# Kernel optimization log

Hardware: AMD Instinct MI355X
Metric: run time of the kernel (lower is better)

The kernel has to match this reference:

```python
import jax, jax.numpy as jnp
import numpy as np

B, S, H, QKV, NH, MLP = 4, 2048, 512, 512, 8, 2048
HD = QKV // NH
EPS = 1e-6


def _layernorm(x):
    # LayerNorm over last dim, no affine, eps=1e-6
    mu = jnp.mean(x, axis=-1, keepdims=True)
    var = jnp.mean(jnp.square(x - mu), axis=-1, keepdims=True)
    return (x - mu) * jax.lax.rsqrt(var + EPS)


def setup_inputs() -> dict:
    key = jax.random.key(0)
    ks = jax.random.split(key, 8)
    sc_in = 1.0 / np.sqrt(H)
    sc_qkv = 1.0 / np.sqrt(QKV)
    sc_mlp = 1.0 / np.sqrt(MLP)
    return {
        "input": jax.random.normal(ks[0], (B, S, H), dtype=jnp.float32),
        "mask": jnp.ones((B, S), dtype=jnp.float32),
        "Wq": jax.random.normal(ks[1], (H, QKV), dtype=jnp.float32) * sc_in,
        "Wk": jax.random.normal(ks[2], (H, QKV), dtype=jnp.float32) * sc_in,
        "Wv": jax.random.normal(ks[3], (H, QKV), dtype=jnp.float32) * sc_in,
        "Wo": jax.random.normal(ks[4], (QKV, H), dtype=jnp.float32) * sc_qkv,
        "W1": jax.random.normal(ks[5], (H, MLP), dtype=jnp.float32) * sc_in,
        "W2": jax.random.normal(ks[6], (MLP, H), dtype=jnp.float32) * sc_mlp,
    }


def reference(input, mask, Wq, Wk, Wv, Wo, W1, W2):
    # pre-mask + pre-norm
    x = input * mask[..., None]
    x = _layernorm(x)
    # qkv projections, split heads: [B,S,QKV] -> [B,NH,S,HD]
    def heads(t):
        return t.reshape(B, S, NH, HD).transpose(0, 2, 1, 3)
    q = heads(x @ Wq) * (1.0 / np.sqrt(HD))
    k = heads(x @ Wk)
    v = heads(x @ Wv)
    logits = jnp.einsum("bhqd,bhkd->bhqk", q, k)  # [B,NH,S,S]
    amask = mask[:, None, :, None]  # 'b q -> b 1 q 1'
    logits = logits + (-100000.0) * (1.0 - amask)
    att = jax.nn.softmax(logits, axis=-1)
    out = jnp.einsum("bhqk,bhkd->bhqd", att, v)
    out = out.transpose(0, 2, 1, 3).reshape(B, S, QKV)
    x = input + out @ Wo  # residual
    x = x * mask[..., None]
    y = _layernorm(x)
    ffn = jax.nn.gelu(y @ W1, approximate=False) @ W2
    return ffn + x
```

## Files before the change

kernel.cpp:

```cpp
#include <hip/hip_runtime.h>
#include <hip/hip_bf16.h>
#include <cmath>

typedef __attribute__((ext_vector_type(8))) short bf16x8;
typedef __attribute__((ext_vector_type(4))) short u16x4;
typedef __attribute__((ext_vector_type(4))) float f32x4;
typedef __attribute__((ext_vector_type(16))) float f32x16;
typedef unsigned short u16;
typedef unsigned int u32;

#define B_ 4
#define S_ 2048
#define H_ 512
#define NH_ 8
#define HD_ 64
#define MLP_ 2048
#define M_ (B_*S_)
#define LOG2E 1.44269504088896340736f

__device__ __forceinline__ float bf2f(u16 u){ u32 v=((u32)u)<<16; float f; __builtin_memcpy(&f,&v,4); return f; }
__device__ __forceinline__ u16 f2bf(float f){ u32 u; __builtin_memcpy(&u,&f,4); u32 r=(u+0x7fffu+((u>>16)&1u))>>16; return (u16)r; }
__device__ __forceinline__ u32 pk2(float lo, float hi2){
  __hip_bfloat162 t = __float22bfloat162_rn(make_float2(lo, hi2));
  u32 r; __builtin_memcpy(&r, &t, 4); return r;
}

__device__ __forceinline__ float xhalf_add(float x){
  float a = x, b = x;
  asm volatile("v_permlane32_swap_b32 %0, %1" : "+v"(a), "+v"(b));
  return a + b;
}

__device__ __forceinline__ void gl16(const u16* g, u16* l) {
  __builtin_amdgcn_global_load_lds((const __attribute__((address_space(1))) u32*)(g),
                                   (__attribute__((address_space(3))) u32*)(l), 16, 0, 0);
}

__device__ __forceinline__ void gemm_core(
    const u16* __restrict__ A, const u16* __restrict__ Bt,
    int lda, int ldb, int nkt, int m0, int n0,
    u16* As, u16* Bs, f32x4 (&acc)[4][4])
{
  const int tid = threadIdx.x;
  const int lane = tid & 63;
  const int w = tid >> 6;
  const int lr = lane & 15;
  const int g  = lane >> 4;
  const int wr = w >> 1, wc = w & 1;

  const int sr = lane >> 3;
  const int scol = ((lane & 7) ^ sr) << 3;

  int aoff[2][4], boff[2][4];
#pragma unroll
  for (int m = 0; m < 4; ++m) {
    int ra = wr*64 + m*16 + lr;
    int rb = wc*64 + m*16 + lr;
#pragma unroll
    for (int kk = 0; kk < 2; ++kk) {
      aoff[kk][m] = ra*64 + (((kk*4+g) ^ (ra&7))<<3);
      boff[kk][m] = rb*64 + (((kk*4+g) ^ (rb&7))<<3);
    }
  }
  const u16* Ap = A + (size_t)m0*lda;
  const u16* Bp = Bt + (size_t)n0*ldb;

#pragma unroll
  for (int c = 0; c < 4; ++c) {
    gl16(Ap + (size_t)(w*32 + c*8 + sr)*lda + scol, As + w*2048 + c*512);
    gl16(Bp + (size_t)(w*32 + c*8 + sr)*ldb + scol, Bs + w*2048 + c*512);
  }

  for (int kt = 0; kt < nkt; ++kt) {
    const int cb = (kt & 1) * 8192;
    if (kt + 1 < nkt) {
      const int k0 = (kt + 1) << 6;
      const int nb = ((kt + 1) & 1) * 8192;
#pragma unroll
      for (int c = 0; c < 4; ++c) {
        gl16(Ap + (size_t)(w*32 + c*8 + sr)*lda + k0 + scol, As + nb + w*2048 + c*512);
        gl16(Bp + (size_t)(w*32 + c*8 + sr)*ldb + k0 + scol, Bs + nb + w*2048 + c*512);
      }
      asm volatile("s_waitcnt vmcnt(8)" ::: "memory");
    } else {
      asm volatile("s_waitcnt vmcnt(0)" ::: "memory");
    }
    __builtin_amdgcn_s_barrier();

#pragma unroll
    for (int kk = 0; kk < 2; ++kk) {
      bf16x8 af[4], bfr[4];
#pragma unroll
      for (int m = 0; m < 4; ++m) {
        af[m]  = *(const bf16x8*)(As + cb + aoff[kk][m]);
        bfr[m] = *(const bf16x8*)(Bs + cb + boff[kk][m]);
      }
#pragma unroll
      for (int m = 0; m < 4; ++m) {
#pragma unroll
        for (int n = 0; n < 4; ++n) {
          acc[m][n] = __builtin_amdgcn_mfma_f32_16x16x32_bf16(af[m], bfr[n], acc[m][n], 0, 0, 0);
        }
      }
    }
    __builtin_amdgcn_s_barrier();
  }
}

__device__ __forceinline__ void gemm_core64(
    const u16* __restrict__ A, const u16* __restrict__ Bt,
    int lda, int ldb, int nkt, int m0, int n0,
    u16* As, u16* Bs, f32x4 (&acc)[2][4])
{
  const int tid = threadIdx.x;
  const int lane = tid & 63;
  const int w = tid >> 6;
  const int lr = lane & 15;
  const int g  = lane >> 4;

  const int sr = lane >> 3;
  const int scol = ((lane & 7) ^ sr) << 3;

  int aoff[2][2], boff[2][4];
#pragma unroll
  for (int m = 0; m < 2; ++m) {
    int ra = w*32 + m*16 + lr;
#pragma unroll
    for (int kk = 0; kk < 2; ++kk) aoff[kk][m] = ra*64 + (((kk*4+g) ^ (ra&7))<<3);
  }
#pragma unroll
  for (int n = 0; n < 4; ++n) {
    int rb = n*16 + lr;
#pragma unroll
    for (int kk = 0; kk < 2; ++kk) boff[kk][n] = rb*64 + (((kk*4+g) ^ (rb&7))<<3);
  }
  const u16* Ap = A + (size_t)m0*lda;
  const u16* Bp = Bt + (size_t)n0*ldb;

#pragma unroll
  for (int c = 0; c < 4; ++c)
    gl16(Ap + (size_t)(w*32 + c*8 + sr)*lda + scol, As + w*2048 + c*512);
#pragma unroll
  for (int c = 0; c < 2; ++c)
    gl16(Bp + (size_t)(w*16 + c*8 + sr)*ldb + scol, Bs + w*1024 + c*512);

  for (int kt = 0; kt < nkt; ++kt) {
    const int cbA = (kt & 1) * 8192;
    const int cbB = (kt & 1) * 4096;
    if (kt + 1 < nkt) {
      const int k0 = (kt + 1) << 6;
      const int nbA = ((kt + 1) & 1) * 8192;
      const int nbB = ((kt + 1) & 1) * 4096;
#pragma unroll
      for (int c = 0; c < 4; ++c)
        gl16(Ap + (size_t)(w*32 + c*8 + sr)*lda + k0 + scol, As + nbA + w*2048 + c*512);
#pragma unroll
      for (int c = 0; c < 2; ++c)
        gl16(Bp + (size_t)(w*16 + c*8 + sr)*ldb + k0 + scol, Bs + nbB + w*1024 + c*512);
      asm volatile("s_waitcnt vmcnt(6)" ::: "memory");
    } else {
      asm volatile("s_waitcnt vmcnt(0)" ::: "memory");
    }
    __builtin_amdgcn_s_barrier();

#pragma unroll
    for (int kk = 0; kk < 2; ++kk) {
      bf16x8 af[2], bfr[4];
#pragma unroll
      for (int m = 0; m < 2; ++m) af[m] = *(const bf16x8*)(As + cbA + aoff[kk][m]);
#pragma unroll
      for (int n = 0; n < 4; ++n) bfr[n] = *(const bf16x8*)(Bs + cbB + boff[kk][n]);
#pragma unroll
      for (int m = 0; m < 2; ++m) {
#pragma unroll
        for (int n = 0; n < 4; ++n) {
          acc[m][n] = __builtin_amdgcn_mfma_f32_16x16x32_bf16(af[m], bfr[n], acc[m][n], 0, 0, 0);
        }
      }
    }
    __builtin_amdgcn_s_barrier();
  }
}

__global__ __launch_bounds__(256,2) void k_qkv(
    const u16* __restrict__ xn, const u16* __restrict__ wqt,
    const u16* __restrict__ wkt, const u16* __restrict__ wvt,
    u16* __restrict__ q, u16* __restrict__ k, u16* __restrict__ vt)
{
  __shared__ u16 As[2*128*64], Bs[2*128*64];
  int m0 = blockIdx.x*128;
  int sel = blockIdx.y >> 2;
  int n0 = (blockIdx.y & 3)*128;
  const u16* Bt = sel==0 ? wqt : (sel==1 ? wkt : wvt);
  float alpha = (sel==0) ? 0.125f*LOG2E : 1.0f;
  f32x4 acc[4][4] = {};
  gemm_core(xn, Bt, H_, H_, H_/64, m0, n0, As, Bs, acc);
  const int lane = threadIdx.x&63, w = threadIdx.x>>6;
  const int lr = lane&15, g = lane>>4, wr = w>>1, wc = w&1;
  if (sel == 2) {
#pragma unroll
    for (int m=0;m<4;++m) {
#pragma unroll
      for (int n=0;n<4;++n) {
        int rowb = m0 + wr*64 + m*16 + g*4;
        int col  = n0 + wc*64 + n*16 + lr;
        int b = rowb >> 11, s = rowb & 2047;
        int h = col >> 6, d = col & 63;
        u16x4 t;
#pragma unroll
        for (int r=0;r<4;++r) t[r] = (short)f2bf(acc[m][n][r]);
        *(u16x4*)(vt + ((size_t)((b*NH_ + h)*HD_ + d))*S_ + s) = t;
      }
    }
  } else {
    u16* O = sel==0 ? q : k;
#pragma unroll
    for (int m=0;m<4;++m) {
#pragma unroll
      for (int n=0;n<4;++n) {
#pragma unroll
        for (int r=0;r<4;++r) {
          int row = m0 + wr*64 + m*16 + g*4 + r;
          int col = n0 + wc*64 + n*16 + lr;
          O[(size_t)row*H_ + col] = f2bf(acc[m][n][r]*alpha);
        }
      }
    }
  }
}

template<int EPI>
__global__ __launch_bounds__(256,2) void k_gemm(
    const u16* __restrict__ A, const u16* __restrict__ Bt, void* __restrict__ Ov,
    const float* __restrict__ aux, const float* __restrict__ maskv,
    int N, int K)
{
  __shared__ u16 As[2*128*64], Bs[2*128*64];
  int m0 = blockIdx.x*128, n0 = blockIdx.y*128;
  f32x4 acc[4][4] = {};
  gemm_core(A, Bt, K, K, K>>6, m0, n0, As, Bs, acc);
  const int lane = threadIdx.x&63, w = threadIdx.x>>6;
  const int lr = lane&15, g = lane>>4, wr = w>>1, wc = w&1;
#pragma unroll
  for (int m=0;m<4;++m) {
#pragma unroll
    for (int n=0;n<4;++n) {
#pragma unroll
      for (int r=0;r<4;++r) {
        int row = m0 + wr*64 + m*16 + g*4 + r;
        int col = n0 + wc*64 + n*16 + lr;
        float val = acc[m][n][r];
        if (EPI == 1) {
          val = 0.5f*val*(1.0f + erff(val*0.70710678118654752f));
          ((u16*)Ov)[(size_t)row*N + col] = f2bf(val);
        } else if (EPI == 2) {
          float mv = maskv[row];
          val = (aux[(size_t)row*N + col] + val)*mv;
          ((float*)Ov)[(size_t)row*N + col] = val;
        } else if (EPI == 3) {
          val += aux[(size_t)row*N + col];
          ((float*)Ov)[(size_t)row*N + col] = val;
        }
      }
    }
  }
}

template<int EPI>
__global__ __launch_bounds__(256,3) void k_gemm64(
    const u16* __restrict__ A, const u16* __restrict__ Bt, void* __restrict__ Ov,
    const float* __restrict__ aux, const float* __restrict__ maskv,
    int N, int K)
{
  __shared__ u16 As[2*128*64], Bs[2*64*64];
  int m0 = blockIdx.x*128, n0 = blockIdx.y*64;
  f32x4 acc[2][4] = {};
  gemm_core64(A, Bt, K, K, K>>6, m0, n0, As, Bs, acc);
  const int lane = threadIdx.x&63, w = threadIdx.x>>6;
  const int lr = lane&15, g = lane>>4;
#pragma unroll
  for (int m=0;m<2;++m) {
#pragma unroll
    for (int n=0;n<4;++n) {
#pragma unroll
      for (int r=0;r<4;++r) {
        int row = m0 + w*32 + m*16 + g*4 + r;
        int col = n0 + n*16 + lr;
        float val = acc[m][n][r];
        if (EPI == 2) {
          float mv = maskv[row];
          val = (aux[(size_t)row*N + col] + val)*mv;
          ((float*)Ov)[(size_t)row*N + col] = val;
        } else if (EPI == 3) {
          val += aux[(size_t)row*N + col];
          ((float*)Ov)[(size_t)row*N + col] = val;
        }
      }
    }
  }
}

template<int MASKED>
__global__ __launch_bounds__(256) void k_ln(const float* __restrict__ in,
    const float* __restrict__ mask, u16* __restrict__ out)
{
  int row = blockIdx.x*4 + (threadIdx.x>>6);
  int lane = threadIdx.x & 63;
  const f32x4* p = (const f32x4*)(in + (size_t)row*H_ + lane*8);
  f32x4 a = p[0], b = p[1];
  float mv = MASKED ? mask[row] : 1.0f;
  float x[8]; float s = 0.f, s2 = 0.f;
#pragma unroll
  for (int j=0;j<4;++j){ x[j] = a[j]*mv; x[4+j] = b[j]*mv; }
#pragma unroll
  for (int j=0;j<8;++j){ s += x[j]; s2 += x[j]*x[j]; }
#pragma unroll
  for (int m=1;m<32;m<<=1){ s += __shfl_xor(s,m); s2 += __shfl_xor(s2,m); }
  s = xhalf_add(s); s2 = xhalf_add(s2);
  float mu = s*(1.0f/H_);
  float var = s2*(1.0f/H_) - mu*mu;
  float inv = rsqrtf(var + 1e-6f);
  bf16x8 o;
#pragma unroll
  for (int j=0;j<8;++j) o[j] = (short)f2bf((x[j]-mu)*inv);
  *(bf16x8*)(out + (size_t)row*H_ + lane*8) = o;
}

__global__ void k_tr4(const float* __restrict__ s0, const float* __restrict__ s1,
                      const float* __restrict__ s2, const float* __restrict__ s3,
                      u16* __restrict__ d0, u16* __restrict__ d1,
                      u16* __restrict__ d2, u16* __restrict__ d3)
{
  __shared__ u16 t[32][33];
  const float* src = blockIdx.z==0 ? s0 : (blockIdx.z==1 ? s1 : (blockIdx.z==2 ? s2 : s3));
  u16* dst = blockIdx.z==0 ? d0 : (blockIdx.z==1 ? d1 : (blockIdx.z==2 ? d2 : d3));
  int c0 = blockIdx.x*32, r0 = blockIdx.y*32;
  int tx = threadIdx.x & 31, ty = threadIdx.x >> 5;
#pragma unroll
  for (int i=0;i<32;i+=8) t[ty+i][tx] = f2bf(src[(size_t)(r0+ty+i)*512 + c0+tx]);
  __syncthreads();
#pragma unroll
  for (int i=0;i<32;i+=8) dst[(size_t)(c0+ty+i)*512 + r0+tx] = t[tx][ty+i];
}

__global__ void k_tr2(const float* __restrict__ W1, const float* __restrict__ W2,
                      u16* __restrict__ d1, u16* __restrict__ d2)
{
  __shared__ u16 t[32][33];
  int z = blockIdx.z;
  const float* src = z ? W2 : W1;
  u16* dst = z ? d2 : d1;
  int R = z ? 2048 : 512;
  int C = z ? 512 : 2048;
  int c0 = (z ? blockIdx.y : blockIdx.x) * 32;
  int r0 = (z ? blockIdx.x : blockIdx.y) * 32;
  int tx = threadIdx.x & 31, ty = threadIdx.x >> 5;
#pragma unroll
  for (int i=0;i<32;i+=8) t[ty+i][tx] = f2bf(src[(size_t)(r0+ty+i)*C + c0+tx]);
  __syncthreads();
#pragma unroll
  for (int i=0;i<32;i+=8) dst[(size_t)(c0+ty+i)*R + r0+tx] = t[tx][ty+i];
}

__global__ __launch_bounds__(256) void k_attn(
    const u16* __restrict__ q, const u16* __restrict__ kmat,
    const u16* __restrict__ vt, const float* __restrict__ mask,
    u16* __restrict__ o)
{
  __shared__ u16 Ks[2][64*64];
  __shared__ u16 Vs[2][64*64];
  __shared__ float bias[S_];
  __shared__ float lsums[4][32];

  const int tid = threadIdx.x;
  const int lane = tid & 63;
  const int w = tid >> 6;
  const int l31 = lane & 31;
  const int hi = lane >> 5;
  const int bh = blockIdx.y, b = bh >> 3, h = bh & 7;
  const int q0 = blockIdx.x * 128;

  const int sr = lane >> 3;
  const int sl = (lane & 7) ^ (sr & 7);
  const u16* ks0 = kmat + (size_t)(b*S_ + w*16 + sr)*H_ + h*HD_ + sl*8;
  const u16* ks1 = ks0 + (size_t)8*H_;
  const u16* vs0 = vt + ((size_t)bh*HD_ + w*16 + sr)*S_ + sl*8;
  const u16* vs1 = vs0 + (size_t)8*S_;

  {
    u16* kd = &Ks[0][0] + w*1024;
    u16* vd = &Vs[0][0] + w*1024;
    gl16(ks0, kd); gl16(ks1, kd + 512);
    gl16(vs0, vd); gl16(vs1, vd + 512);
  }

  for (int j = tid; j < S_; j += 256) bias[j] = -144269.5f * (1.0f - mask[b*S_ + j]);

  bf16x8 qf[4];
  {
    const u16* qp = q + (size_t)(b*S_ + q0 + w*32 + l31)*H_ + h*HD_ + hi*8;
#pragma unroll
    for (int ds = 0; ds < 4; ++ds) qf[ds] = *(const bf16x8*)(qp + ds*16);
  }

  f32x16 po0 = {}, po1 = {};
  float mreg = -1e30f, lsum = 0.f;

  __syncthreads();

  for (int jt = 0; jt < 32; ++jt) {
    const int buf = jt & 1;
    if (jt < 31) {
      const int j0 = (jt + 1) * 64;
      u16* kd = &Ks[buf ^ 1][0] + w*1024;
      u16* vd = &Vs[buf ^ 1][0] + w*1024;
      gl16(ks0 + (size_t)j0*H_, kd); gl16(ks1 + (size_t)j0*H_, kd + 512);
      gl16(vs0 + j0, vd);            gl16(vs1 + j0, vd + 512);
      asm volatile("s_waitcnt vmcnt(4)" ::: "memory");
    } else {
      asm volatile("s_waitcnt vmcnt(0)" ::: "memory");
    }
    __builtin_amdgcn_s_barrier();

    const u16* kt  = &Ks[buf][0];
    const u16* vtl = &Vs[buf][0];

    f32x16 s0, s1;
    const float* bp = &bias[jt*64 + hi*4];
#pragma unroll
    for (int kb = 0; kb < 2; ++kb) {
      f32x16 acc;
#pragma unroll
      for (int g2 = 0; g2 < 4; ++g2) {
        f32x4 b4 = *(const f32x4*)(bp + kb*32 + g2*8);
        acc[g2*4+0] = b4[0]; acc[g2*4+1] = b4[1];
        acc[g2*4+2] = b4[2]; acc[g2*4+3] = b4[3];
      }
      const int key = kb*32 + l31;
      const u16* kr = kt + key*64;
      __builtin_amdgcn_s_setprio(1);
#pragma unroll
      for (int ds = 0; ds < 4; ++ds) {
        bf16x8 kf = *(const bf16x8*)(kr + (((ds*2 + hi) ^ (key & 7)) << 3));
        acc = __builtin_amdgcn_mfma_f32_32x32x16_bf16(kf, qf[ds], acc, 0, 0, 0);
      }
      __builtin_amdgcn_s_setprio(0);
      if (kb == 0) s0 = acc; else s1 = acc;
    }

    float mx = s0[0];
#pragma unroll
    for (int r = 1; r < 16; ++r) mx = fmaxf(mx, s0[r]);
#pragma unroll
    for (int r = 0; r < 16; ++r) mx = fmaxf(mx, s1[r]);
    mx = fmaxf(mx, __shfl_xor(mx, 32));
    if (__any(mx > mreg + 8.0f)) {
      float mn = fmaxf(mreg, mx);
      float sc = __builtin_amdgcn_exp2f(mreg - mn);
      lsum *= sc;
#pragma unroll
      for (int r = 0; r < 16; ++r) { po0[r] *= sc; po1[r] *= sc; }
      mreg = mn;
    }
    float ps = 0.f;
#pragma unroll
    for (int r = 0; r < 16; ++r) { float p = __builtin_amdgcn_exp2f(s0[r]-mreg); s0[r] = p; ps += p; }
#pragma unroll
    for (int r = 0; r < 16; ++r) { float p = __builtin_amdgcn_exp2f(s1[r]-mreg); s1[r] = p; ps += p; }
    ps += __shfl_xor(ps, 32);
    lsum += ps;

#pragma unroll
    for (int kb = 0; kb < 2; ++kb) {
      const f32x16& sv = kb ? s1 : s0;
      u32 w01 = pk2(sv[0],  sv[1]);
      u32 w23 = pk2(sv[2],  sv[3]);
      u32 w45 = pk2(sv[4],  sv[5]);
      u32 w67 = pk2(sv[6],  sv[7]);
      asm volatile("v_permlane32_swap_b32 %0, %1" : "+v"(w01), "+v"(w45));
      asm volatile("v_permlane32_swap_b32 %0, %1" : "+v"(w23), "+v"(w67));
      u32 w89 = pk2(sv[8],  sv[9]);
      u32 wab = pk2(sv[10], sv[11]);
      u32 wcd = pk2(sv[12], sv[13]);
      u32 wef = pk2(sv[14], sv[15]);
      asm volatile("v_permlane32_swap_b32 %0, %1" : "+v"(w89), "+v"(wcd));
      asm volatile("v_permlane32_swap_b32 %0, %1" : "+v"(wab), "+v"(wef));
      union { u32 wrd[4]; bf16x8 v; } f0, f1;
      f0.wrd[0]=w01; f0.wrd[1]=w23; f0.wrd[2]=w45; f0.wrd[3]=w67;
      f1.wrd[0]=w89; f1.wrd[1]=wab; f1.wrd[2]=wcd; f1.wrd[3]=wef;
      __builtin_amdgcn_s_setprio(1);
#pragma unroll
      for (int ks = 0; ks < 2; ++ks) {
        bf16x8 pa = ks ? f1.v : f0.v;
#pragma unroll
        for (int nb = 0; nb < 2; ++nb) {
          int dd = nb*32 + l31;
          int slot = ((kb*4 + ks*2 + hi) ^ (dd & 7)) << 3;
          bf16x8 vf = *(const bf16x8*)(vtl + dd*64 + slot);
          if (nb == 0) po0 = __builtin_amdgcn_mfma_f32_32x32x16_bf16(pa, vf, po0, 0,0,0);
          else         po1 = __builtin_amdgcn_mfma_f32_32x32x16_bf16(pa, vf, po1, 0,0,0);
        }
      }
      __builtin_amdgcn_s_setprio(0);
    }
    __builtin_amdgcn_s_barrier();
  }

  if (hi == 0) lsums[w][l31] = lsum;
  f32x4 li[4];
#pragma unroll
  for (int g2i = 0; g2i < 4; ++g2i) {
    f32x4 t = *(const f32x4*)&lsums[w][g2i*8 + hi*4];
    li[g2i][0] = 1.0f/t[0]; li[g2i][1] = 1.0f/t[1];
    li[g2i][2] = 1.0f/t[2]; li[g2i][3] = 1.0f/t[3];
  }
  u16* op = o + (size_t)(b*S_ + q0 + w*32)*H_ + h*HD_;
#pragma unroll
  for (int nb = 0; nb < 2; ++nb) {
#pragma unroll
    for (int r = 0; r < 16; ++r) {
      int row = (r&3) + 8*(r>>2) + 4*hi;
      float val = (nb ? po1[r] : po0[r]) * li[r>>2][r&3];
      op[(size_t)row*H_ + nb*32 + l31] = f2bf(val);
    }
  }
}

extern "C" void kernel_launch(void* const* d_in, const int* in_sizes, int n_in,
                              void* d_out, int out_size, void* d_ws, size_t ws_size,
                              hipStream_t stream) {
  const float* input = (const float*)d_in[0];
  const float* mask  = (const float*)d_in[1];
  const float* Wq = (const float*)d_in[2];
  const float* Wk = (const float*)d_in[3];
  const float* Wv = (const float*)d_in[4];
  const float* Wo = (const float*)d_in[5];
  const float* W1 = (const float*)d_in[6];
  const float* W2 = (const float*)d_in[7];
  float* out = (float*)d_out;
  u16* ws = (u16*)d_ws;

  u16* wqt = ws;
  u16* wkt = wqt + 262144;
  u16* wvt = wkt + 262144;
  u16* wot = wvt + 262144;
  u16* w1t = wot + 262144;
  u16* w2t = w1t + 1048576;
  u16* xn  = w2t + 1048576;
  u16* q   = xn  + 4194304;
  u16* k   = q   + 4194304;
  u16* v   = k   + 4194304;
  u16* vt  = v   + 4194304;
  u16*   attn = xn;
  float* x2f  = (float*)q;
  u16*   y    = v;
  u16*   h1   = vt;

  dim3 blk(256);
  k_tr4<<<dim3(16,16,4), blk, 0, stream>>>(Wq, Wk, Wv, Wo, wqt, wkt, wvt, wot);
  k_tr2<<<dim3(64,16,2), blk, 0, stream>>>(W1, W2, w1t, w2t);

  k_ln<1><<<2048, blk, 0, stream>>>(input, mask, xn);
  k_qkv<<<dim3(64,12), blk, 0, stream>>>(xn, wqt, wkt, wvt, q, k, vt);
  k_attn<<<dim3(16,32), blk, 0, stream>>>(q, k, vt, mask, attn);
  k_gemm64<2><<<dim3(64,8), blk, 0, stream>>>(attn, wot, (void*)x2f, input, mask, 512, 512);
  k_ln<0><<<2048, blk, 0, stream>>>(x2f, nullptr, y);
  k_gemm<1><<<dim3(64,16), blk, 0, stream>>>(y, w1t, (void*)h1, nullptr, nullptr, 2048, 512);
  k_gemm64<3><<<dim3(64,8), blk, 0, stream>>>(h1, w2t, (void*)out, x2f, nullptr, 512, 2048);
}
```

Before: 184.2 us.

## Fuse weight transposes and first layernorm; add XCD-aware block swizzle to GEMMs

```diff
diff --git a/kernel.cpp b/kernel.cpp
--- a/kernel.cpp
+++ b/kernel.cpp
@@ -36,6 +36,13 @@
                                    (__attribute__((address_space(3))) u32*)(l), 16, 0, 0);
 }
 
+__device__ __forceinline__ void swz_mn(int* mt, int* nt) {
+  int lin = blockIdx.x + 64*blockIdx.y;
+  int xcd = lin & 7, idx = lin >> 3;
+  *mt = xcd*8 + (idx & 7);
+  *nt = idx >> 3;
+}
+
 __device__ __forceinline__ void gemm_core(
     const u16* __restrict__ A, const u16* __restrict__ Bt,
     int lda, int ldb, int nkt, int m0, int n0,
@@ -188,9 +195,10 @@
     u16* __restrict__ q, u16* __restrict__ k, u16* __restrict__ vt)
 {
   __shared__ u16 As[2*128*64], Bs[2*128*64];
-  int m0 = blockIdx.x*128;
-  int sel = blockIdx.y >> 2;
-  int n0 = (blockIdx.y & 3)*128;
+  int mt, nt; swz_mn(&mt, &nt);
+  int m0 = mt*128;
+  int sel = nt >> 2;
+  int n0 = (nt & 3)*128;
   const u16* Bt = sel==0 ? wqt : (sel==1 ? wkt : wvt);
   float alpha = (sel==0) ? 0.125f*LOG2E : 1.0f;
   f32x4 acc[4][4] = {};
@@ -236,7 +244,8 @@
     int N, int K)
 {
   __shared__ u16 As[2*128*64], Bs[2*128*64];
-  int m0 = blockIdx.x*128, n0 = blockIdx.y*128;
+  int mt, nt; swz_mn(&mt, &nt);
+  int m0 = mt*128, n0 = nt*128;
   f32x4 acc[4][4] = {};
   gemm_core(A, Bt, K, K, K>>6, m0, n0, As, Bs, acc);
   const int lane = threadIdx.x&63, w = threadIdx.x>>6;
@@ -273,7 +282,8 @@
     int N, int K)
 {
   __shared__ u16 As[2*128*64], Bs[2*64*64];
-  int m0 = blockIdx.x*128, n0 = blockIdx.y*64;
+  int mt, nt; swz_mn(&mt, &nt);
+  int m0 = mt*128, n0 = nt*64;
   f32x4 acc[2][4] = {};
   gemm_core64(A, Bt, K, K, K>>6, m0, n0, As, Bs, acc);
   const int lane = threadIdx.x&63, w = threadIdx.x>>6;
@@ -326,40 +336,65 @@
   *(bf16x8*)(out + (size_t)row*H_ + lane*8) = o;
 }
 
-__global__ void k_tr4(const float* __restrict__ s0, const float* __restrict__ s1,
-                      const float* __restrict__ s2, const float* __restrict__ s3,
-                      u16* __restrict__ d0, u16* __restrict__ d1,
-                      u16* __restrict__ d2, u16* __restrict__ d3)
+__global__ __launch_bounds__(256) void k_pre(
+    const float* __restrict__ Wq, const float* __restrict__ Wk,
+    const float* __restrict__ Wv, const float* __restrict__ Wo,
+    const float* __restrict__ W1, const float* __restrict__ W2,
+    u16* __restrict__ wqt, u16* __restrict__ wkt, u16* __restrict__ wvt,
+    u16* __restrict__ wot, u16* __restrict__ w1t, u16* __restrict__ w2t,
+    const float* __restrict__ input, const float* __restrict__ mask,
+    u16* __restrict__ xn)
 {
   __shared__ u16 t[32][33];
-  const float* src = blockIdx.z==0 ? s0 : (blockIdx.z==1 ? s1 : (blockIdx.z==2 ? s2 : s3));
-  u16* dst = blockIdx.z==0 ? d0 : (blockIdx.z==1 ? d1 : (blockIdx.z==2 ? d2 : d3));
-  int c0 = blockIdx.x*32, r0 = blockIdx.y*32;
-  int tx = threadIdx.x & 31, ty = threadIdx.x >> 5;
-#pragma unroll
-  for (int i=0;i<32;i+=8) t[ty+i][tx] = f2bf(src[(size_t)(r0+ty+i)*512 + c0+tx]);
-  __syncthreads();
-#pragma unroll
-  for (int i=0;i<32;i+=8) dst[(size_t)(c0+ty+i)*512 + r0+tx] = t[tx][ty+i];
-}
-
-__global__ void k_tr2(const float* __restrict__ W1, const float* __restrict__ W2,
-                      u16* __restrict__ d1, u16* __restrict__ d2)
-{
-  __shared__ u16 t[32][33];
-  int z = blockIdx.z;
-  const float* src = z ? W2 : W1;
-  u16* dst = z ? d2 : d1;
-  int R = z ? 2048 : 512;
-  int C = z ? 512 : 2048;
-  int c0 = (z ? blockIdx.y : blockIdx.x) * 32;
-  int r0 = (z ? blockIdx.x : blockIdx.y) * 32;
-  int tx = threadIdx.x & 31, ty = threadIdx.x >> 5;
-#pragma unroll
-  for (int i=0;i<32;i+=8) t[ty+i][tx] = f2bf(src[(size_t)(r0+ty+i)*C + c0+tx]);
-  __syncthreads();
-#pragma unroll
-  for (int i=0;i<32;i+=8) dst[(size_t)(c0+ty+i)*R + r0+tx] = t[tx][ty+i];
+  const int id = blockIdx.x;
+  const int tx = threadIdx.x & 31, ty = threadIdx.x >> 5;
+
+  if (id < 1024) {
+    int z = id >> 8, tt = id & 255;
+    const float* src = z==0?Wq : z==1?Wk : z==2?Wv : Wo;
+    u16* dst = z==0?wqt : z==1?wkt : z==2?wvt : wot;
+    int c0 = (tt & 15)*32, r0 = (tt >> 4)*32;
+#pragma unroll
+    for (int i=0;i<32;i+=8) t[ty+i][tx] = f2bf(src[(size_t)(r0+ty+i)*512 + c0+tx]);
+    __syncthreads();
+#pragma unroll
+    for (int i=0;i<32;i+=8) dst[(size_t)(c0+ty+i)*512 + r0+tx] = t[tx][ty+i];
+  } else if (id < 3072) {
+    int z = (id-1024) >> 10, tt = (id-1024) & 1023;
+    const float* src = z ? W2 : W1;
+    u16* dst = z ? w2t : w1t;
+    int R = z ? 2048 : 512;
+    int C = z ? 512 : 2048;
+    int a = tt & 63, bq = tt >> 6;
+    int c0 = (z ? bq : a)*32;
+    int r0 = (z ? a : bq)*32;
+#pragma unroll
+    for (int i=0;i<32;i+=8) t[ty+i][tx] = f2bf(src[(size_t)(r0+ty+i)*C + c0+tx]);
+    __syncthreads();
+#pragma unroll
+    for (int i=0;i<32;i+=8) dst[(size_t)(c0+ty+i)*R + r0+tx] = t[tx][ty+i];
+  } else {
+    int row = (id-3072)*4 + (threadIdx.x>>6);
+    int lane = threadIdx.x & 63;
+    const f32x4* p = (const f32x4*)(input + (size_t)row*H_ + lane*8);
+    f32x4 a = p[0], b = p[1];
+    float mv = mask[row];
+    float x[8]; float s = 0.f, s2 = 0.f;
+#pragma unroll
+    for (int j=0;j<4;++j){ x[j] = a[j]*mv; x[4+j] = b[j]*mv; }
+#pragma unroll
+    for (int j=0;j<8;++j){ s += x[j]; s2 += x[j]*x[j]; }
+#pragma unroll
+    for (int m=1;m<32;m<<=1){ s += __shfl_xor(s,m); s2 += __shfl_xor(s2,m); }
+    s = xhalf_add(s); s2 = xhalf_add(s2);
+    float mu = s*(1.0f/H_);
+    float var = s2*(1.0f/H_) - mu*mu;
+    float inv = rsqrtf(var + 1e-6f);
+    bf16x8 o;
+#pragma unroll
+    for (int j=0;j<8;++j) o[j] = (short)f2bf((x[j]-mu)*inv);
+    *(bf16x8*)(xn + (size_t)row*H_ + lane*8) = o;
+  }
 }
 
 __global__ __launch_bounds__(256) void k_attn(
@@ -557,10 +592,9 @@
   u16*   h1   = vt;
 
   dim3 blk(256);
-  k_tr4<<<dim3(16,16,4), blk, 0, stream>>>(Wq, Wk, Wv, Wo, wqt, wkt, wvt, wot);
-  k_tr2<<<dim3(64,16,2), blk, 0, stream>>>(W1, W2, w1t, w2t);
-
-  k_ln<1><<<2048, blk, 0, stream>>>(input, mask, xn);
+  k_pre<<<dim3(5120), blk, 0, stream>>>(Wq, Wk, Wv, Wo, W1, W2,
+                                        wqt, wkt, wvt, wot, w1t, w2t,
+                                        input, mask, xn);
   k_qkv<<<dim3(64,12), blk, 0, stream>>>(xn, wqt, wkt, wvt, q, k, vt);
   k_attn<<<dim3(16,32), blk, 0, stream>>>(q, k, vt, mask, attn);
   k_gemm64<2><<<dim3(64,8), blk, 0, stream>>>(attn, wot, (void*)x2f, input, mask, 512, 512);
```

Result: faster. 179.3 us (-2.7%).
